# Performance work log

Hardware: AMD Instinct MI355X
Metric: run time of the kernel (lower is better)

Reference implementation:

```python
import jax, jax.numpy as jnp
import numpy as np

N, B, FIN, FOUT = 4096, 16, 128, 128
DENSITY = 0.01


def setup_inputs() -> dict:
    key = jax.random.key(0)
    k1, k2, k3, k4 = jax.random.split(key, 4)
    # sparse binary adjacency (static pattern), stored dense for the reference
    adj = (jax.random.uniform(k1, (N, N)) < DENSITY).astype(jnp.float32)
    x = jax.random.normal(k2, (B, N, FIN), dtype=jnp.float32)
    W = jax.random.normal(k3, (FOUT, FIN), dtype=jnp.float32) * (1.0 / np.sqrt(FIN))
    b = jax.random.normal(k4, (FOUT,), dtype=jnp.float32) * 0.01
    return {"adj": adj, "x": x, "W": W, "b": b}


def _normalized_adj(adj):
    # A_hat = D^{-1/2} (A + I) D^{-1/2}, degrees from column sums (dim=0 in torch)
    a_self = adj + jnp.eye(adj.shape[0], dtype=adj.dtype)
    dinv = jax.lax.rsqrt(jnp.sum(a_self, axis=0))
    return dinv[:, None] * a_self * dinv[None, :]


def reference(adj, x, W, b):
    a_norm = _normalized_adj(adj)
    # SpMM aggregation over nodes: (N,N) x (B,N,F) -> (B,N,F)
    agg = jnp.einsum('nm,bmf->bnf', a_norm, x)
    # dense linear transform: fc(agg)
    return jnp.einsum('bnf,of->bno', agg, W) + b
```

## Files before the change

kernel.cpp:

```cpp
#include <hip/hip_runtime.h>


#define NN 4096
#define FD 128
#define NB 16
#define CAP 96
#define CPAD 104
#define XB 512

typedef float     f32x4 __attribute__((ext_vector_type(4)));
typedef _Float16  f16x4 __attribute__((ext_vector_type(4)));
typedef _Float16  f16x8 __attribute__((ext_vector_type(8)));
typedef int       i32x2 __attribute__((ext_vector_type(2)));
typedef int       i32x4 __attribute__((ext_vector_type(4)));

#define XP 136

__device__ __forceinline__ float fmamix_lo(float acc, int pk, float w) {
    asm("v_fma_mix_f32 %0, %1, %2, %0 op_sel:[0,0,0] op_sel_hi:[1,0,0]"
        : "+v"(acc) : "v"(pk), "v"(w));
    return acc;
}
__device__ __forceinline__ float fmamix_hi(float acc, int pk, float w) {
    asm("v_fma_mix_f32 %0, %1, %2, %0 op_sel:[1,0,0] op_sel_hi:[1,0,0]"
        : "+v"(acc) : "v"(pk), "v"(w));
    return acc;
}

__global__ __launch_bounds__(256) void k_bx(const float* __restrict__ A,
                                            float* __restrict__ deg,
                                            int* __restrict__ cnt,
                                            unsigned short* __restrict__ csr,
                                            const float* __restrict__ x,
                                            const float* __restrict__ W,
                                            _Float16* __restrict__ y) {
    __shared__ __align__(16) char smem[FD * XP * 2];
    const int t = threadIdx.x;

    if (blockIdx.x < XB) {
        _Float16 (*sW)[XP] = (_Float16(*)[XP])smem;
        const size_t rbase = (size_t)blockIdx.x * 128;

        #pragma unroll
        for (int i = 0; i < 8; ++i) {
            const int id = t + i * 256;
            const int o = id >> 4, f8 = (id & 15) * 8;
            const f32x4 a = *(const f32x4*)&W[(size_t)o * FD + f8];
            const f32x4 b = *(const f32x4*)&W[(size_t)o * FD + f8 + 4];
            f16x8 h;
            h[0]=(_Float16)a.x; h[1]=(_Float16)a.y; h[2]=(_Float16)a.z; h[3]=(_Float16)a.w;
            h[4]=(_Float16)b.x; h[5]=(_Float16)b.y; h[6]=(_Float16)b.z; h[7]=(_Float16)b.w;
            *(f16x8*)&sW[o][f8] = h;
        }
        __syncthreads();

        const int w = t >> 6, lane = t & 63;
        const int lrow = lane & 15, koct = (lane >> 4) * 8;
        const float* xr0 = x + (rbase + w * 32 + lrow) * FD;
        const float* xr1 = xr0 + 16 * FD;
        f32x4 acc[2][8] = {};
        #pragma unroll
        for (int kc = 0; kc < 4; ++kc) {
            const int ko = kc * 32 + koct;
            const f32x4 a0 = *(const f32x4*)&xr0[ko];
            const f32x4 a1 = *(const f32x4*)&xr0[ko + 4];
            const f32x4 b0 = *(const f32x4*)&xr1[ko];
            const f32x4 b1 = *(const f32x4*)&xr1[ko + 4];
            f16x8 xx0, xx1;
            xx0[0]=(_Float16)a0.x; xx0[1]=(_Float16)a0.y; xx0[2]=(_Float16)a0.z; xx0[3]=(_Float16)a0.w;
            xx0[4]=(_Float16)a1.x; xx0[5]=(_Float16)a1.y; xx0[6]=(_Float16)a1.z; xx0[7]=(_Float16)a1.w;
            xx1[0]=(_Float16)b0.x; xx1[1]=(_Float16)b0.y; xx1[2]=(_Float16)b0.z; xx1[3]=(_Float16)b0.w;
            xx1[4]=(_Float16)b1.x; xx1[5]=(_Float16)b1.y; xx1[6]=(_Float16)b1.z; xx1[7]=(_Float16)b1.w;
            #pragma unroll
            for (int ot = 0; ot < 8; ++ot) {
                const f16x8 ww = *(const f16x8*)&sW[ot * 16 + lrow][ko];
                acc[0][ot] = __builtin_amdgcn_mfma_f32_16x16x32_f16(ww, xx0, acc[0][ot], 0, 0, 0);
                acc[1][ot] = __builtin_amdgcn_mfma_f32_16x16x32_f16(ww, xx1, acc[1][ot], 0, 0, 0);
            }
        }
        #pragma unroll
        for (int rt = 0; rt < 2; ++rt) {
            const size_t row = rbase + w * 32 + rt * 16 + (lane & 15);
            #pragma unroll
            for (int ot = 0; ot < 8; ++ot) {
                f16x4 h;
                h[0] = (_Float16)acc[rt][ot][0];
                h[1] = (_Float16)acc[rt][ot][1];
                h[2] = (_Float16)acc[rt][ot][2];
                h[3] = (_Float16)acc[rt][ot][3];
                *(f16x4*)&y[row * FD + ot * 16 + (lane >> 4) * 4] = h;
            }
        }
        return;
    }

    int* sCnt = (int*)smem;
    const int n = blockIdx.x - XB;
    const float* row = A + (size_t)n * NN + t * 16;
    float r[16];
    *(f32x4*)&r[0]  = ((const f32x4*)row)[0];
    *(f32x4*)&r[4]  = ((const f32x4*)row)[1];
    *(f32x4*)&r[8]  = ((const f32x4*)row)[2];
    *(f32x4*)&r[12] = ((const f32x4*)row)[3];

    int c = 0;
    #pragma unroll
    for (int j = 0; j < 16; ++j) c += (r[j] != 0.0f) ? 1 : 0;
    sCnt[t] = c;
    __syncthreads();
    for (int off = 1; off < 256; off <<= 1) {
        const int v = sCnt[t];
        const int u = (t >= off) ? sCnt[t - off] : 0;
        __syncthreads();
        sCnt[t] = v + u;
        __syncthreads();
    }
    int pos = sCnt[t] - c;
    #pragma unroll
    for (int j = 0; j < 16; ++j) {
        if (r[j] != 0.0f) {
            const int m = t * 16 + j;
            if (pos < CAP) csr[(size_t)n * CAP + pos] = (unsigned short)m;
            ++pos;
            atomicAdd(&deg[m], 1.0f);
        }
    }
    if (t == 255) {
        int tot = sCnt[255];
        cnt[n] = tot < CAP ? tot : CAP;
    }
}

__global__ __launch_bounds__(256) void k_agg2(const _Float16* __restrict__ y,
                                              const int* __restrict__ cnt,
                                              const unsigned short* __restrict__ csr,
                                              const float* __restrict__ deg,
                                              const float* __restrict__ bias,
                                              float* __restrict__ out) {
    __shared__ int sL[4][CPAD * 2];
    const int t = threadIdx.x, w = t >> 6, lane = t & 63;
    const int bid = blockIdx.x;
    const int xcd = bid & 7;
    const int b0  = 2 * xcd;
    const int n   = (bid >> 3) * 4 + w;
    const int c = cnt[n];
    const int totPad = (c + 1 + 3) & ~3;

    for (int k = lane; k < CPAD; k += 64) {
        int m; float wv;
        if (k < c)       { m = csr[(size_t)n * CAP + k]; wv = rsqrtf(1.0f + deg[m]); }
        else if (k == c) { m = n; wv = rsqrtf(1.0f + deg[n]); }
        else             { m = n; wv = 0.0f; }
        sL[w][2 * k]     = m << 8;
        sL[w][2 * k + 1] = __float_as_int(wv);
    }
    __syncthreads();

    const int rq = lane >> 4;
    const int fo = (lane & 15) * 16;
    const char* yb0 = (const char*)y + (size_t)b0 * (NN * FD * 2);
    const char* yb1 = yb0 + (size_t)(NN * FD * 2);

    float acc0[8] = {}, acc1[8] = {};
    #pragma unroll 2
    for (int k = rq; k < totPad; k += 4) {
        const i32x2 e = *(const i32x2*)&sL[w][2 * k];
        const unsigned v = (unsigned)(e.x + fo);
        const i32x4 pA = *(const i32x4*)(yb0 + v);
        const i32x4 pB = *(const i32x4*)(yb1 + v);
        const float wt = __int_as_float(e.y);
        #pragma unroll
        for (int j = 0; j < 4; ++j) {
            acc0[2*j]   = fmamix_lo(acc0[2*j],   pA[j], wt);
            acc0[2*j+1] = fmamix_hi(acc0[2*j+1], pA[j], wt);
            acc1[2*j]   = fmamix_lo(acc1[2*j],   pB[j], wt);
            acc1[2*j+1] = fmamix_hi(acc1[2*j+1], pB[j], wt);
        }
    }

    #pragma unroll
    for (int j = 0; j < 8; ++j) {
        acc0[j] += __shfl_xor(acc0[j], 16);
        acc0[j] += __shfl_xor(acc0[j], 32);
        acc1[j] += __shfl_xor(acc1[j], 16);
        acc1[j] += __shfl_xor(acc1[j], 32);
    }

    if (lane < 32) {
        const float dn = rsqrtf(1.0f + deg[n]);
        const int h = lane >> 4;
        const int f0 = (lane & 15) * 8 + h * 4;
        const f32x4 bb = *(const f32x4*)(bias + f0);
        f32x4 o0, o1;
        o0.x = acc0[h * 4 + 0] * dn + bb.x;
        o0.y = acc0[h * 4 + 1] * dn + bb.y;
        o0.z = acc0[h * 4 + 2] * dn + bb.z;
        o0.w = acc0[h * 4 + 3] * dn + bb.w;
        o1.x = acc1[h * 4 + 0] * dn + bb.x;
        o1.y = acc1[h * 4 + 1] * dn + bb.y;
        o1.z = acc1[h * 4 + 2] * dn + bb.z;
        o1.w = acc1[h * 4 + 3] * dn + bb.w;
        f32x4* d0 = (f32x4*)(out + ((size_t)b0 * NN + n) * FD + f0);
        f32x4* d1 = (f32x4*)(out + ((size_t)(b0 + 1) * NN + n) * FD + f0);
        __builtin_nontemporal_store(o0, d0);
        __builtin_nontemporal_store(o1, d1);
    }
}

extern "C" void kernel_launch(void* const* d_in, const int* in_sizes, int n_in,
                              void* d_out, int out_size, void* d_ws, size_t ws_size,
                              hipStream_t stream) {
    const float* A    = (const float*)d_in[0];
    const float* x    = (const float*)d_in[1];
    const float* W    = (const float*)d_in[2];
    const float* bias = (const float*)d_in[3];
    float* out = (float*)d_out;

    float*          deg  = (float*)d_ws;
    int*            cnt  = (int*)((char*)d_ws + 2 * NN * 4);
    unsigned short* csr  = (unsigned short*)(cnt + NN);
    _Float16*       y    = (_Float16*)((char*)d_ws + (3 * NN * 4 + (size_t)NN * CAP * 2));

    hipMemsetAsync(deg, 0, NN * sizeof(float), stream);
    k_bx  <<<XB + NN, 256, 0, stream>>>(A, deg, cnt, csr, x, W, y);
    k_agg2<<<(NN / 4) * (NB / 2), 256, 0, stream>>>(y, cnt, csr, deg, bias, out);
}
```

Measured before the change: 74.44 us.

## Build CSR for two rows per block with wave-shuffle prefix scan

The CSR-building part of k_bx now handles two adjacency rows per block, with both counts packed into one int as 16-bit halves, and the launch grid shrinks to match. The shared-memory Hillis-Steele scan with many __syncthreads is replaced by an intra-wave shuffle scan plus a small cross-wave sum needing one barrier. This targets the barrier overhead and block count of the dense-adjacency scan. Packing is safe because per-row counts stay below 65536, but each thread now holds twice as many loaded values.

```diff
diff --git a/kernel.cpp b/kernel.cpp
--- a/kernel.cpp
+++ b/kernel.cpp
@@ -94,40 +94,62 @@
         return;
     }
 
-    int* sCnt = (int*)smem;
-    const int n = blockIdx.x - XB;
-    const float* row = A + (size_t)n * NN + t * 16;
-    float r[16];
-    *(f32x4*)&r[0]  = ((const f32x4*)row)[0];
-    *(f32x4*)&r[4]  = ((const f32x4*)row)[1];
-    *(f32x4*)&r[8]  = ((const f32x4*)row)[2];
-    *(f32x4*)&r[12] = ((const f32x4*)row)[3];
-
-    int c = 0;
-    #pragma unroll
-    for (int j = 0; j < 16; ++j) c += (r[j] != 0.0f) ? 1 : 0;
-    sCnt[t] = c;
+    int* sWsum = (int*)smem;
+    const int w = t >> 6, lane = t & 63;
+    const int n0 = (blockIdx.x - XB) * 2;
+    const float* row0 = A + (size_t)n0 * NN + t * 16;
+    const float* row1 = row0 + NN;
+    float r0[16], r1[16];
+    *(f32x4*)&r0[0]  = ((const f32x4*)row0)[0];
+    *(f32x4*)&r0[4]  = ((const f32x4*)row0)[1];
+    *(f32x4*)&r0[8]  = ((const f32x4*)row0)[2];
+    *(f32x4*)&r0[12] = ((const f32x4*)row0)[3];
+    *(f32x4*)&r1[0]  = ((const f32x4*)row1)[0];
+    *(f32x4*)&r1[4]  = ((const f32x4*)row1)[1];
+    *(f32x4*)&r1[8]  = ((const f32x4*)row1)[2];
+    *(f32x4*)&r1[12] = ((const f32x4*)row1)[3];
+
+    int c0 = 0, c1 = 0;
+    #pragma unroll
+    for (int j = 0; j < 16; ++j) {
+        c0 += (r0[j] != 0.0f) ? 1 : 0;
+        c1 += (r1[j] != 0.0f) ? 1 : 0;
+    }
+    const int own = c0 | (c1 << 16);
+
+    int s = own;
+    #pragma unroll
+    for (int off = 1; off < 64; off <<= 1) {
+        const int u = __shfl(s, lane - off);
+        s += (lane >= off) ? u : 0;
+    }
+    if (lane == 63) sWsum[w] = s;
     __syncthreads();
-    for (int off = 1; off < 256; off <<= 1) {
-        const int v = sCnt[t];
-        const int u = (t >= off) ? sCnt[t - off] : 0;
-        __syncthreads();
-        sCnt[t] = v + u;
-        __syncthreads();
-    }
-    int pos = sCnt[t] - c;
+    int wbase = 0;
+    #pragma unroll
+    for (int j = 0; j < 4; ++j) wbase += (j < w) ? sWsum[j] : 0;
+
+    const int base = wbase + s - own;
+    int pos0 = base & 0xffff, pos1 = base >> 16;
     #pragma unroll
     for (int j = 0; j < 16; ++j) {
-        if (r[j] != 0.0f) {
-            const int m = t * 16 + j;
-            if (pos < CAP) csr[(size_t)n * CAP + pos] = (unsigned short)m;
-            ++pos;
+        const int m = t * 16 + j;
+        if (r0[j] != 0.0f) {
+            if (pos0 < CAP) csr[(size_t)n0 * CAP + pos0] = (unsigned short)m;
+            ++pos0;
             atomicAdd(&deg[m], 1.0f);
         }
+        if (r1[j] != 0.0f) {
+            if (pos1 < CAP) csr[(size_t)(n0 + 1) * CAP + pos1] = (unsigned short)m;
+            ++pos1;
+            atomicAdd(&deg[m], 1.0f);
+        }
     }
     if (t == 255) {
-        int tot = sCnt[255];
-        cnt[n] = tot < CAP ? tot : CAP;
+        const int tot = wbase + s;
+        const int t0 = tot & 0xffff, t1 = tot >> 16;
+        cnt[n0]     = t0 < CAP ? t0 : CAP;
+        cnt[n0 + 1] = t1 < CAP ? t1 : CAP;
     }
 }
 
@@ -222,6 +244,6 @@
     _Float16*       y    = (_Float16*)((char*)d_ws + (3 * NN * 4 + (size_t)NN * CAP * 2));
 
     hipMemsetAsync(deg, 0, NN * sizeof(float), stream);
-    k_bx  <<<XB + NN, 256, 0, stream>>>(A, deg, cnt, csr, x, W, y);
+    k_bx  <<<XB + NN / 2, 256, 0, stream>>>(A, deg, cnt, csr, x, W, y);
     k_agg2<<<(NN / 4) * (NB / 2), 256, 0, stream>>>(y, cnt, csr, deg, bias, out);
 }
```

Result: slower. 76.59 us (+2.9%).
